# Kernel optimization log

Measured on AMD Instinct MI355X. Metric: run time of the kernel, lower is better.

The kernel has to match this reference:

```python
import jax, jax.numpy as jnp
import numpy as np

N_HEADS = 16
HEAD_DIM = 64
ROPE_BASE = 10000.0


def _rope_cos_sin(T, d, dtype):
    # GPT-NeoX style: inv_freq over even indices, cos/sin duplicated to full head_dim
    inv_freq = 1.0 / (ROPE_BASE ** (jnp.arange(0, d, 2, dtype=jnp.float32) / d))
    freqs = jnp.arange(T, dtype=jnp.float32)[:, None] * inv_freq[None, :]  # [T, d/2]
    emb = jnp.concatenate([freqs, freqs], axis=-1)  # [T, d]
    return jnp.cos(emb).astype(dtype), jnp.sin(emb).astype(dtype)


def _rotate_half(x):
    x1, x2 = jnp.split(x, 2, axis=-1)
    return jnp.concatenate([-x2, x1], axis=-1)


def setup_inputs() -> dict:
    key = jax.random.key(0)
    k1, k2, k3 = jax.random.split(key, 3)
    B, T, C = 2, 2048, 1024
    x = jax.random.normal(k1, (B, T, C), dtype=jnp.float32)
    Wqkv = jax.random.normal(k2, (C, 3 * C), dtype=jnp.float32) * (1.0 / np.sqrt(C))
    Wout = jax.random.normal(k3, (C, C), dtype=jnp.float32) * (1.0 / np.sqrt(C))
    return {"x": x, "Wqkv": Wqkv, "Wout": Wout}


def reference(x, Wqkv, Wout):
    B, T, C = x.shape
    H, D = N_HEADS, HEAD_DIM
    qkv = (x @ Wqkv).reshape(B, T, 3, H, D)
    q, k, v = qkv[:, :, 0], qkv[:, :, 1], qkv[:, :, 2]  # [B,T,H,D]
    q = q.transpose(0, 2, 1, 3)  # [B,H,T,D]
    k = k.transpose(0, 2, 1, 3)
    v = v.transpose(0, 2, 1, 3)
    cos, sin = _rope_cos_sin(T, D, x.dtype)  # [T,D]
    cos = cos[None, None]
    sin = sin[None, None]
    q = q * cos + _rotate_half(q) * sin
    k = k * cos + _rotate_half(k) * sin
    scale = 1.0 / np.sqrt(D)
    scores = jnp.einsum("bhqd,bhkd->bhqk", q, k) * scale  # [B,H,T,T]
    causal = jnp.tril(jnp.ones((T, T), dtype=bool))
    scores = jnp.where(causal[None, None], scores, jnp.finfo(scores.dtype).min)
    attn = jax.nn.softmax(scores, axis=-1)
    out = jnp.einsum("bhqk,bhkd->bhqd", attn, v)  # [B,H,T,D]
    out = out.transpose(0, 2, 1, 3).reshape(B, T, C)
    return out @ Wout
```

## Files before the change

kernel.cpp:

```cpp
#include <hip/hip_runtime.h>


#define B_  2
#define T_  2048
#define C_  1024
#define H_  16
#define D_  64
#define N3_ 3072

typedef unsigned short ushortx8 __attribute__((ext_vector_type(8)));
typedef unsigned short ushortx4 __attribute__((ext_vector_type(4)));
typedef short bf16x8 __attribute__((ext_vector_type(8)));
typedef float f32x4 __attribute__((ext_vector_type(4)));
typedef float f32x16 __attribute__((ext_vector_type(16)));
typedef unsigned int uintx2 __attribute__((ext_vector_type(2)));

__device__ __forceinline__ unsigned short f2bf(float f) {
  union { float f; unsigned u; } v; v.f = f;
  unsigned r = v.u + 0x7FFFu + ((v.u >> 16) & 1u);
  return (unsigned short)(r >> 16);
}
__device__ __forceinline__ float bf2f(unsigned short h) {
  union { unsigned u; float f; } v; v.u = ((unsigned)h) << 16;
  return v.f;
}
__device__ __forceinline__ unsigned cvtpk_bf16(float lo, float hi) {
  unsigned r; asm("v_cvt_pk_bf16_f32 %0, %1, %2" : "=v"(r) : "v"(lo), "v"(hi));
  return r;
}
__device__ __forceinline__ void gload_lds16(const void* g, void* l) {
  __builtin_amdgcn_global_load_lds((const __attribute__((address_space(1))) void*)g,
                                   (__attribute__((address_space(3))) void*)l,
                                   16, 0, 0);
}

__global__ __launch_bounds__(256) void prep_kernel(const float* __restrict__ x,
                                                   unsigned short* __restrict__ Xb,
                                                   const float* __restrict__ Wqkv,
                                                   unsigned short* __restrict__ WqkvT,
                                                   const float* __restrict__ Wout,
                                                   unsigned short* __restrict__ WoutT) {
  __shared__ float tile[32][33];
  const int bid = blockIdx.x;
  if (bid < 4096) {
    size_t i = ((size_t)bid * 256 + threadIdx.x) * 4;
    const float4 v = *(const float4*)(x + i);
    ushortx4 o;
    o[0] = f2bf(v.x); o[1] = f2bf(v.y); o[2] = f2bf(v.z); o[3] = f2bf(v.w);
    *(ushortx4*)(Xb + i) = o;
    return;
  }
  const float* W;
  unsigned short* WT;
  int K, N, n0, k0;
  if (bid < 7168) {
    const int idx = bid - 4096;
    W = Wqkv; WT = WqkvT; K = C_; N = N3_;
    n0 = (idx % (N3_ / 32)) * 32; k0 = (idx / (N3_ / 32)) * 32;
  } else {
    const int idx = bid - 7168;
    W = Wout; WT = WoutT; K = C_; N = C_;
    n0 = (idx % (C_ / 32)) * 32; k0 = (idx / (C_ / 32)) * 32;
  }
  const int tx = threadIdx.x & 31, ty = threadIdx.x >> 5;
#pragma unroll
  for (int i = 0; i < 4; ++i)
    tile[ty + i * 8][tx] = W[(size_t)(k0 + ty + i * 8) * N + n0 + tx];
  __syncthreads();
#pragma unroll
  for (int i = 0; i < 4; ++i)
    WT[(size_t)(n0 + ty + i * 8) * K + k0 + tx] = f2bf(tile[tx][ty + i * 8]);
}

template <int OUTF32>
__global__ __launch_bounds__(256) void gemm_bt_kernel(const unsigned short* __restrict__ A,
                                                      const unsigned short* __restrict__ BT,
                                                      void* __restrict__ Cptr,
                                                      int M, int N, int K) {
  __shared__ unsigned short Alds[128 * 64];
  __shared__ unsigned short Blds[128 * 64];
  const int tid = threadIdx.x;
  const int w = tid >> 6, l = tid & 63;
  const int wr = w >> 1, wc = w & 1;
  const int lg = l >> 4, lr = l & 15;
  const int m0 = blockIdx.y * 128, n0 = blockIdx.x * 128;
  const int lr8 = l >> 3;
  const int lc8 = (l & 7) ^ lr8;

  f32x4 acc[4][4];
#pragma unroll
  for (int i = 0; i < 4; ++i)
#pragma unroll
    for (int j = 0; j < 4; ++j) acc[i][j] = f32x4{0.f, 0.f, 0.f, 0.f};

  for (int k0 = 0; k0 < K; k0 += 64) {
    __syncthreads();
#pragma unroll
    for (int i = 0; i < 4; ++i) {
      const int ch = w * 4 + i;
      gload_lds16(A + (size_t)(m0 + ch * 8 + lr8) * K + k0 + lc8 * 8, &Alds[ch * 512]);
      gload_lds16(BT + (size_t)(n0 + ch * 8 + lr8) * K + k0 + lc8 * 8, &Blds[ch * 512]);
    }
    __syncthreads();
#pragma unroll
    for (int kc = 0; kc < 2; ++kc) {
      bf16x8 af[4], bfr[4];
#pragma unroll
      for (int mi = 0; mi < 4; ++mi) {
        const int row = wr * 64 + mi * 16 + lr;
        const int c16 = (kc * 4 + lg) ^ (row & 7);
        af[mi] = *(const bf16x8*)(&Alds[row * 64 + c16 * 8]);
      }
#pragma unroll
      for (int nj = 0; nj < 4; ++nj) {
        const int row = wc * 64 + nj * 16 + lr;
        const int c16 = (kc * 4 + lg) ^ (row & 7);
        bfr[nj] = *(const bf16x8*)(&Blds[row * 64 + c16 * 8]);
      }
#pragma unroll
      for (int mi = 0; mi < 4; ++mi)
#pragma unroll
        for (int nj = 0; nj < 4; ++nj)
          acc[mi][nj] = __builtin_amdgcn_mfma_f32_16x16x32_bf16(af[mi], bfr[nj], acc[mi][nj], 0, 0, 0);
    }
  }
#pragma unroll
  for (int mi = 0; mi < 4; ++mi)
#pragma unroll
    for (int nj = 0; nj < 4; ++nj)
#pragma unroll
      for (int j = 0; j < 4; ++j) {
        const int row = m0 + wr * 64 + mi * 16 + lg * 4 + j;
        const int col = n0 + wc * 64 + nj * 16 + lr;
        if (OUTF32) ((float*)Cptr)[(size_t)row * N + col] = acc[mi][nj][j];
        else ((unsigned short*)Cptr)[(size_t)row * N + col] = f2bf(acc[mi][nj][j]);
      }
}

__global__ __launch_bounds__(256) void rope_vtrans_kernel(const unsigned short* __restrict__ QKV,
                                                          unsigned short* __restrict__ Qp,
                                                          unsigned short* __restrict__ Kp,
                                                          unsigned short* __restrict__ Vt) {
  __shared__ unsigned short tile[64][72];
  const int tt = blockIdx.x, bh = blockIdx.y;
  const int b = bh >> 4, h = bh & 15;
  const int tid = threadIdx.x;
  if (blockIdx.z == 0) {
    const int half = tid >> 7;
    const int r = (tid >> 1) & 63;
    const int d0 = (tid & 1) * 16;
    const int t = tt * 64 + r;
    const unsigned short* src = QKV + (size_t)(b * T_ + t) * N3_ + half * C_ + h * D_;
    ushortx8 lo0 = *(const ushortx8*)(src + d0);
    ushortx8 lo1 = *(const ushortx8*)(src + d0 + 8);
    ushortx8 hi0 = *(const ushortx8*)(src + d0 + 32);
    ushortx8 hi1 = *(const ushortx8*)(src + d0 + 40);
    ushortx8 olo0, olo1, ohi0, ohi1;
    const float scale = half ? 1.0f : 0.18033688011112042f;
    const float tf = (float)t;
#pragma unroll
    for (int jj = 0; jj < 16; ++jj) {
      const int d = d0 + jj;
      const float invf = exp2f((float)d * -0.41524101186092036f);
      const float ang = tf * invf;
      const float c = cosf(ang), s = sinf(ang);
      const float xl = bf2f(jj < 8 ? lo0[jj] : lo1[jj - 8]);
      const float xh = bf2f(jj < 8 ? hi0[jj] : hi1[jj - 8]);
      const unsigned short rl = f2bf((xl * c - xh * s) * scale);
      const unsigned short rh = f2bf((xh * c + xl * s) * scale);
      if (jj < 8) { olo0[jj] = rl; ohi0[jj] = rh; }
      else        { olo1[jj - 8] = rl; ohi1[jj - 8] = rh; }
    }
    unsigned short* dst = (half ? Kp : Qp) + ((size_t)bh * T_ + t) * D_;
    *(ushortx8*)(dst + d0) = olo0;
    *(ushortx8*)(dst + d0 + 8) = olo1;
    *(ushortx8*)(dst + d0 + 32) = ohi0;
    *(ushortx8*)(dst + d0 + 40) = ohi1;
  } else {
    {
      const int r = tid >> 2, seg = tid & 3;
      const unsigned short* src = QKV + (size_t)(b * T_ + tt * 64 + r) * N3_ + 2 * C_ + h * D_ + seg * 16;
      *(ushortx8*)(&tile[r][seg * 16]) = *(const ushortx8*)(src);
      *(ushortx8*)(&tile[r][seg * 16 + 8]) = *(const ushortx8*)(src + 8);
    }
    __syncthreads();
    {
      const int d = tid >> 2, ts = tid & 3;
      ushortx8 o0, o1;
#pragma unroll
      for (int i = 0; i < 8; ++i) { o0[i] = tile[ts * 16 + i][d]; o1[i] = tile[ts * 16 + 8 + i][d]; }
      unsigned short* dst = Vt + ((size_t)bh * D_ + d) * T_ + tt * 64 + ts * 16;
      *(ushortx8*)(dst) = o0;
      *(ushortx8*)(dst + 8) = o1;
    }
  }
}

__global__ __launch_bounds__(256, 2) void attn9_kernel(const unsigned short* __restrict__ Qp,
                                                       const unsigned short* __restrict__ Kp,
                                                       const unsigned short* __restrict__ Vt,
                                                       unsigned short* __restrict__ Ob) {
  __shared__ unsigned short Klds[3][64 * 64];
  __shared__ unsigned short Vlds[3][64 * 64];
  const int tid = threadIdx.x, w = tid >> 6, l = tid & 63;
  const int lq = l & 31, hi = l >> 5;
  const int swz = lq & 7;
  const int bid = blockIdx.x;
  const int bh = bid & 31;
  const int j = bid >> 5;
  const int g = (j < 8) ? (15 - j) : (j - 8);
  const int s = 4 * g + w;
  const int q0 = s * 32;
  const int ntiles = 2 * g + 2;
  const size_t koff = (size_t)bh * T_ * D_;
  const unsigned short* Kb = Kp + koff;
  const unsigned short* Vb = Vt + (size_t)bh * D_ * T_;

  const int lr8 = l >> 3;
  const int lc8 = (l & 7) ^ lr8;

  bf16x8 qf[4];
  {
    const unsigned short* qp = Qp + koff + (size_t)(q0 + lq) * D_ + hi * 8;
#pragma unroll
    for (int ds = 0; ds < 4; ++ds) qf[ds] = *(const bf16x8*)(qp + ds * 16);
  }
  f32x16 o0, o1;
#pragma unroll
  for (int r = 0; r < 16; ++r) { o0[r] = 0.f; o1[r] = 0.f; }
  float m = -3.0e38f, lden = 0.f;

#pragma unroll
  for (int i = 0; i < 2; ++i) {
    const int c = w * 2 + i;
    gload_lds16(Kb + (size_t)(c * 8 + lr8) * D_ + lc8 * 8, &Klds[0][c * 512]);
    gload_lds16(Vb + (size_t)(c * 8 + lr8) * T_ + lc8 * 8, &Vlds[0][c * 512]);
  }

  for (int kt = 0; kt < ntiles; ++kt) {
    const int cur = kt % 3;
    const int nxt = (kt + 1) % 3;
    const int ktn = (kt + 1 < ntiles) ? kt + 1 : kt;
    const int kvn = ktn * 64;
#pragma unroll
    for (int i = 0; i < 2; ++i) {
      const int c = w * 2 + i;
      gload_lds16(Kb + (size_t)(kvn + c * 8 + lr8) * D_ + lc8 * 8, &Klds[nxt][c * 512]);
      gload_lds16(Vb + (size_t)(c * 8 + lr8) * T_ + kvn + lc8 * 8, &Vlds[nxt][c * 512]);
    }
    asm volatile("s_waitcnt vmcnt(4)" ::: "memory");
    __builtin_amdgcn_s_barrier();
    __builtin_amdgcn_sched_barrier(0);

    const int kv0 = kt * 64;
    if (kv0 <= q0 + 31) {
      const unsigned short* KL = &Klds[cur][0];
      const unsigned short* VL = &Vlds[cur][0];
      f32x16 acc0, acc1;
#pragma unroll
      for (int r = 0; r < 16; ++r) { acc0[r] = 0.f; acc1[r] = 0.f; }
      __builtin_amdgcn_s_setprio(1);
#pragma unroll
      for (int ds = 0; ds < 4; ++ds) {
        const int slot = ((ds * 2 + hi) ^ swz) * 8;
        const bf16x8 kf0 = *(const bf16x8*)(&KL[(lq) * 64 + slot]);
        const bf16x8 kf1 = *(const bf16x8*)(&KL[(32 + lq) * 64 + slot]);
        acc0 = __builtin_amdgcn_mfma_f32_32x32x16_bf16(kf0, qf[ds], acc0, 0, 0, 0);
        acc1 = __builtin_amdgcn_mfma_f32_32x32x16_bf16(kf1, qf[ds], acc1, 0, 0, 0);
      }
      __builtin_amdgcn_s_setprio(0);
      if (kv0 + 63 > q0) {
        const int thr0 = q0 + lq - kv0;
        const int thr1 = thr0 - 32;
#pragma unroll
        for (int r = 0; r < 16; ++r) {
          const int kvloc = (r & 3) + 8 * (r >> 2) + 4 * hi;
          if (kvloc > thr0) acc0[r] = -3.0e38f;
          if (kvloc > thr1) acc1[r] = -3.0e38f;
        }
      }
      float mx[8];
#pragma unroll
      for (int i = 0; i < 8; ++i)
        mx[i] = fmaxf(fmaxf(acc0[i], acc0[i + 8]), fmaxf(acc1[i], acc1[i + 8]));
#pragma unroll
      for (int i = 0; i < 4; ++i) mx[i] = fmaxf(mx[i], mx[i + 4]);
      const float mloc = fmaxf(fmaxf(mx[0], mx[1]), fmaxf(mx[2], mx[3]));
      const uintx2 mp = __builtin_amdgcn_permlane32_swap(__float_as_uint(mloc), __float_as_uint(mloc), false, false);
      const float pm = fmaxf(__uint_as_float(mp.x), __uint_as_float(mp.y));
      const bool grow = pm > m + 8.0f;
      if (__any(grow)) {
        const float mn = grow ? pm : m;
        const float alpha = __builtin_amdgcn_exp2f(m - mn);
        m = mn;
        lden *= alpha;
#pragma unroll
        for (int r = 0; r < 16; ++r) { o0[r] *= alpha; o1[r] *= alpha; }
      }
      float p0[16], p1[16];
#pragma unroll
      for (int r = 0; r < 16; ++r) {
        p0[r] = __builtin_amdgcn_exp2f(acc0[r] - m);
        p1[r] = __builtin_amdgcn_exp2f(acc1[r] - m);
      }
      unsigned W0 = cvtpk_bf16(p0[0], p0[1]), W1 = cvtpk_bf16(p0[2], p0[3]);
      unsigned W2 = cvtpk_bf16(p0[4], p0[5]), W3 = cvtpk_bf16(p0[6], p0[7]);
      uintx2 Aa = __builtin_amdgcn_permlane32_swap(W0, W2, false, false);
      uintx2 Ab = __builtin_amdgcn_permlane32_swap(W1, W3, false, false);
      union { unsigned u[4]; bf16x8 v; } pfa0 = {{Aa.x, Ab.x, Aa.y, Ab.y}};
      W0 = cvtpk_bf16(p0[8], p0[9]);   W1 = cvtpk_bf16(p0[10], p0[11]);
      W2 = cvtpk_bf16(p0[12], p0[13]); W3 = cvtpk_bf16(p0[14], p0[15]);
      Aa = __builtin_amdgcn_permlane32_swap(W0, W2, false, false);
      Ab = __builtin_amdgcn_permlane32_swap(W1, W3, false, false);
      union { unsigned u[4]; bf16x8 v; } pfa1 = {{Aa.x, Ab.x, Aa.y, Ab.y}};
      W0 = cvtpk_bf16(p1[0], p1[1]);   W1 = cvtpk_bf16(p1[2], p1[3]);
      W2 = cvtpk_bf16(p1[4], p1[5]);   W3 = cvtpk_bf16(p1[6], p1[7]);
      Aa = __builtin_amdgcn_permlane32_swap(W0, W2, false, false);
      Ab = __builtin_amdgcn_permlane32_swap(W1, W3, false, false);
      union { unsigned u[4]; bf16x8 v; } pfb0 = {{Aa.x, Ab.x, Aa.y, Ab.y}};
      W0 = cvtpk_bf16(p1[8], p1[9]);   W1 = cvtpk_bf16(p1[10], p1[11]);
      W2 = cvtpk_bf16(p1[12], p1[13]); W3 = cvtpk_bf16(p1[14], p1[15]);
      Aa = __builtin_amdgcn_permlane32_swap(W0, W2, false, false);
      Ab = __builtin_amdgcn_permlane32_swap(W1, W3, false, false);
      union { unsigned u[4]; bf16x8 v; } pfb1 = {{Aa.x, Ab.x, Aa.y, Ab.y}};

      __builtin_amdgcn_s_setprio(1);
#pragma unroll
      for (int dt = 0; dt < 2; ++dt) {
        const int rowb = (dt * 32 + lq) * 64;
        const bf16x8 vf0 = *(const bf16x8*)(&VL[rowb + ((0 * 2 + hi) ^ swz) * 8]);
        const bf16x8 vf1 = *(const bf16x8*)(&VL[rowb + ((1 * 2 + hi) ^ swz) * 8]);
        const bf16x8 vf2 = *(const bf16x8*)(&VL[rowb + ((2 * 2 + hi) ^ swz) * 8]);
        const bf16x8 vf3 = *(const bf16x8*)(&VL[rowb + ((3 * 2 + hi) ^ swz) * 8]);
        if (dt == 0) {
          o0 = __builtin_amdgcn_mfma_f32_32x32x16_bf16(vf0, pfa0.v, o0, 0, 0, 0);
          o0 = __builtin_amdgcn_mfma_f32_32x32x16_bf16(vf1, pfa1.v, o0, 0, 0, 0);
          o0 = __builtin_amdgcn_mfma_f32_32x32x16_bf16(vf2, pfb0.v, o0, 0, 0, 0);
          o0 = __builtin_amdgcn_mfma_f32_32x32x16_bf16(vf3, pfb1.v, o0, 0, 0, 0);
        } else {
          o1 = __builtin_amdgcn_mfma_f32_32x32x16_bf16(vf0, pfa0.v, o1, 0, 0, 0);
          o1 = __builtin_amdgcn_mfma_f32_32x32x16_bf16(vf1, pfa1.v, o1, 0, 0, 0);
          o1 = __builtin_amdgcn_mfma_f32_32x32x16_bf16(vf2, pfb0.v, o1, 0, 0, 0);
          o1 = __builtin_amdgcn_mfma_f32_32x32x16_bf16(vf3, pfb1.v, o1, 0, 0, 0);
        }
      }
      __builtin_amdgcn_s_setprio(0);
      float sm[8];
#pragma unroll
      for (int i = 0; i < 8; ++i) sm[i] = (p0[i] + p0[i + 8]) + (p1[i] + p1[i + 8]);
#pragma unroll
      for (int i = 0; i < 4; ++i) sm[i] = sm[i] + sm[i + 4];
      const float sloc = (sm[0] + sm[1]) + (sm[2] + sm[3]);
      const uintx2 sp = __builtin_amdgcn_permlane32_swap(__float_as_uint(sloc), __float_as_uint(sloc), false, false);
      lden += __uint_as_float(sp.x) + __uint_as_float(sp.y);
    }
  }
  asm volatile("s_waitcnt vmcnt(0)" ::: "memory");

  const float rl = __builtin_amdgcn_rcpf(lden);
  const int b = bh >> 4, hh = bh & 15;
  unsigned short* orow = Ob + (size_t)(b * T_ + q0 + lq) * C_ + hh * D_ + 4 * hi;
#pragma unroll
  for (int rq = 0; rq < 4; ++rq) {
    ushortx4 ov0, ov1;
#pragma unroll
    for (int i = 0; i < 4; ++i) {
      ov0[i] = f2bf(o0[rq * 4 + i] * rl);
      ov1[i] = f2bf(o1[rq * 4 + i] * rl);
    }
    *(ushortx4*)(orow + rq * 8) = ov0;
    *(ushortx4*)(orow + 32 + rq * 8) = ov1;
  }
}

extern "C" void kernel_launch(void* const* d_in, const int* in_sizes, int n_in,
                              void* d_out, int out_size, void* d_ws, size_t ws_size,
                              hipStream_t stream) {
  const float* x = (const float*)d_in[0];
  const float* Wqkv = (const float*)d_in[1];
  const float* Wout = (const float*)d_in[2];
  float* out = (float*)d_out;
  char* ws = (char*)d_ws;
  unsigned short* Xb    = (unsigned short*)(ws);
  unsigned short* WqkvT = (unsigned short*)(ws + (8ull << 20));
  unsigned short* WoutT = (unsigned short*)(ws + (14ull << 20));
  unsigned short* QKVb  = (unsigned short*)(ws + (16ull << 20));
  unsigned short* Qp    = (unsigned short*)(ws + (40ull << 20));
  unsigned short* Kp    = (unsigned short*)(ws + (48ull << 20));
  unsigned short* Vt    = (unsigned short*)(ws + (56ull << 20));
  unsigned short* Ob    = (unsigned short*)(ws + (64ull << 20));

  prep_kernel<<<8192, 256, 0, stream>>>(x, Xb, Wqkv, WqkvT, Wout, WoutT);
  gemm_bt_kernel<0><<<dim3(N3_ / 128, (B_ * T_) / 128), 256, 0, stream>>>(
      Xb, WqkvT, QKVb, B_ * T_, N3_, C_);
  rope_vtrans_kernel<<<dim3(T_ / 64, B_ * H_, 2), 256, 0, stream>>>(QKVb, Qp, Kp, Vt);
  attn9_kernel<<<512, 256, 0, stream>>>(Qp, Kp, Vt, Ob);
  gemm_bt_kernel<1><<<dim3(C_ / 128, (B_ * T_) / 128), 256, 0, stream>>>(
      Ob, WoutT, out, B_ * T_, C_, C_);
}
```

Before: 118.4 us.

## Widen attention KV tiles to 128 with double-buffered LDS staging

The attention kernel now processes 128 keys per iteration instead of 64, with four score accumulators and eight PV MFMAs per step. LDS goes from triple-buffered 64-wide tiles to double-buffered 128-wide tiles, with a new XOR swizzle for the V tile and an extra barrier before each prefetch. This halves the number of loop iterations, softmax reductions and barriers, but drops the per-wave skip of fully masked tiles. Waves whose queries sit early in a 128-key tile now do some wasted masked compute, and register pressure rises.

```diff
diff --git a/kernel.cpp b/kernel.cpp
--- a/kernel.cpp
+++ b/kernel.cpp
@@ -196,12 +196,12 @@
   }
 }
 
-__global__ __launch_bounds__(256, 2) void attn9_kernel(const unsigned short* __restrict__ Qp,
-                                                       const unsigned short* __restrict__ Kp,
-                                                       const unsigned short* __restrict__ Vt,
-                                                       unsigned short* __restrict__ Ob) {
-  __shared__ unsigned short Klds[3][64 * 64];
-  __shared__ unsigned short Vlds[3][64 * 64];
+__global__ __launch_bounds__(256, 2) void attn10_kernel(const unsigned short* __restrict__ Qp,
+                                                        const unsigned short* __restrict__ Kp,
+                                                        const unsigned short* __restrict__ Vt,
+                                                        unsigned short* __restrict__ Ob) {
+  __shared__ unsigned short Klds[2][128 * 64];
+  __shared__ unsigned short Vlds[2][64 * 128];
   const int tid = threadIdx.x, w = tid >> 6, l = tid & 63;
   const int lq = l & 31, hi = l >> 5;
   const int swz = lq & 7;
@@ -209,15 +209,16 @@
   const int bh = bid & 31;
   const int j = bid >> 5;
   const int g = (j < 8) ? (15 - j) : (j - 8);
-  const int s = 4 * g + w;
-  const int q0 = s * 32;
-  const int ntiles = 2 * g + 2;
+  const int q0 = (4 * g + w) * 32;
+  const int nt = g + 1;
   const size_t koff = (size_t)bh * T_ * D_;
   const unsigned short* Kb = Kp + koff;
   const unsigned short* Vb = Vt + (size_t)bh * D_ * T_;
 
   const int lr8 = l >> 3;
   const int lc8 = (l & 7) ^ lr8;
+  const int vrl = l >> 4;
+  const int vsl = l & 15;
 
   bf16x8 qf[4];
   {
@@ -230,130 +231,148 @@
   for (int r = 0; r < 16; ++r) { o0[r] = 0.f; o1[r] = 0.f; }
   float m = -3.0e38f, lden = 0.f;
 
-#pragma unroll
-  for (int i = 0; i < 2; ++i) {
-    const int c = w * 2 + i;
-    gload_lds16(Kb + (size_t)(c * 8 + lr8) * D_ + lc8 * 8, &Klds[0][c * 512]);
-    gload_lds16(Vb + (size_t)(c * 8 + lr8) * T_ + lc8 * 8, &Vlds[0][c * 512]);
-  }
-
-  for (int kt = 0; kt < ntiles; ++kt) {
-    const int cur = kt % 3;
-    const int nxt = (kt + 1) % 3;
-    const int ktn = (kt + 1 < ntiles) ? kt + 1 : kt;
-    const int kvn = ktn * 64;
-#pragma unroll
-    for (int i = 0; i < 2; ++i) {
-      const int c = w * 2 + i;
-      gload_lds16(Kb + (size_t)(kvn + c * 8 + lr8) * D_ + lc8 * 8, &Klds[nxt][c * 512]);
-      gload_lds16(Vb + (size_t)(c * 8 + lr8) * T_ + kvn + lc8 * 8, &Vlds[nxt][c * 512]);
-    }
-    asm volatile("s_waitcnt vmcnt(4)" ::: "memory");
+  auto stage = [&](int buf, int kv0s) {
+#pragma unroll
+    for (int i = 0; i < 4; ++i) {
+      const int c = w * 4 + i;
+      gload_lds16(Kb + (size_t)(kv0s + c * 8 + lr8) * D_ + lc8 * 8, &Klds[buf][c * 512]);
+    }
+#pragma unroll
+    for (int i = 0; i < 4; ++i) {
+      const int c = w * 4 + i;
+      const int vr = c * 4 + vrl;
+      const int vs = vsl ^ (vr & 7);
+      gload_lds16(Vb + (size_t)vr * T_ + kv0s + vs * 8, &Vlds[buf][c * 512]);
+    }
+  };
+  auto pack2 = [&](const f32x16& p, bf16x8& fa, bf16x8& fb) {
+    unsigned W0 = cvtpk_bf16(p[0], p[1]), W1 = cvtpk_bf16(p[2], p[3]);
+    unsigned W2 = cvtpk_bf16(p[4], p[5]), W3 = cvtpk_bf16(p[6], p[7]);
+    uintx2 Aa = __builtin_amdgcn_permlane32_swap(W0, W2, false, false);
+    uintx2 Ab = __builtin_amdgcn_permlane32_swap(W1, W3, false, false);
+    union { unsigned u[4]; bf16x8 v; } t1 = {{Aa.x, Ab.x, Aa.y, Ab.y}};
+    fa = t1.v;
+    W0 = cvtpk_bf16(p[8], p[9]);   W1 = cvtpk_bf16(p[10], p[11]);
+    W2 = cvtpk_bf16(p[12], p[13]); W3 = cvtpk_bf16(p[14], p[15]);
+    Aa = __builtin_amdgcn_permlane32_swap(W0, W2, false, false);
+    Ab = __builtin_amdgcn_permlane32_swap(W1, W3, false, false);
+    union { unsigned u[4]; bf16x8 v; } t2 = {{Aa.x, Ab.x, Aa.y, Ab.y}};
+    fb = t2.v;
+  };
+
+  stage(0, 0);
+
+  for (int kt = 0; kt < nt; ++kt) {
+    const int cur = kt & 1, nxt = cur ^ 1;
+    __builtin_amdgcn_s_barrier();
+    const int ktn = (kt + 1 < nt) ? kt + 1 : kt;
+    stage(nxt, ktn * 128);
+    asm volatile("s_waitcnt vmcnt(8)" ::: "memory");
     __builtin_amdgcn_s_barrier();
     __builtin_amdgcn_sched_barrier(0);
 
-    const int kv0 = kt * 64;
-    if (kv0 <= q0 + 31) {
-      const unsigned short* KL = &Klds[cur][0];
-      const unsigned short* VL = &Vlds[cur][0];
-      f32x16 acc0, acc1;
-#pragma unroll
-      for (int r = 0; r < 16; ++r) { acc0[r] = 0.f; acc1[r] = 0.f; }
-      __builtin_amdgcn_s_setprio(1);
-#pragma unroll
-      for (int ds = 0; ds < 4; ++ds) {
-        const int slot = ((ds * 2 + hi) ^ swz) * 8;
-        const bf16x8 kf0 = *(const bf16x8*)(&KL[(lq) * 64 + slot]);
-        const bf16x8 kf1 = *(const bf16x8*)(&KL[(32 + lq) * 64 + slot]);
-        acc0 = __builtin_amdgcn_mfma_f32_32x32x16_bf16(kf0, qf[ds], acc0, 0, 0, 0);
-        acc1 = __builtin_amdgcn_mfma_f32_32x32x16_bf16(kf1, qf[ds], acc1, 0, 0, 0);
+    const unsigned short* KL = &Klds[cur][0];
+    const unsigned short* VL = &Vlds[cur][0];
+    const int kv0 = kt * 128;
+    f32x16 a0, a1, a2, a3;
+#pragma unroll
+    for (int r = 0; r < 16; ++r) { a0[r] = 0.f; a1[r] = 0.f; a2[r] = 0.f; a3[r] = 0.f; }
+    __builtin_amdgcn_s_setprio(1);
+#pragma unroll
+    for (int ds = 0; ds < 4; ++ds) {
+      const int slot = ((ds * 2 + hi) ^ swz) * 8;
+      const bf16x8 k0f = *(const bf16x8*)(&KL[(lq) * 64 + slot]);
+      const bf16x8 k1f = *(const bf16x8*)(&KL[(32 + lq) * 64 + slot]);
+      const bf16x8 k2f = *(const bf16x8*)(&KL[(64 + lq) * 64 + slot]);
+      const bf16x8 k3f = *(const bf16x8*)(&KL[(96 + lq) * 64 + slot]);
+      a0 = __builtin_amdgcn_mfma_f32_32x32x16_bf16(k0f, qf[ds], a0, 0, 0, 0);
+      a1 = __builtin_amdgcn_mfma_f32_32x32x16_bf16(k1f, qf[ds], a1, 0, 0, 0);
+      a2 = __builtin_amdgcn_mfma_f32_32x32x16_bf16(k2f, qf[ds], a2, 0, 0, 0);
+      a3 = __builtin_amdgcn_mfma_f32_32x32x16_bf16(k3f, qf[ds], a3, 0, 0, 0);
+    }
+    __builtin_amdgcn_s_setprio(0);
+    if (kv0 + 127 > q0) {
+      const int thr = q0 + lq - kv0;
+#pragma unroll
+      for (int r = 0; r < 16; ++r) {
+        const int kvloc = (r & 3) + 8 * (r >> 2) + 4 * hi;
+        if (kvloc > thr)      a0[r] = -3.0e38f;
+        if (kvloc > thr - 32) a1[r] = -3.0e38f;
+        if (kvloc > thr - 64) a2[r] = -3.0e38f;
+        if (kvloc > thr - 96) a3[r] = -3.0e38f;
       }
-      __builtin_amdgcn_s_setprio(0);
-      if (kv0 + 63 > q0) {
-        const int thr0 = q0 + lq - kv0;
-        const int thr1 = thr0 - 32;
-#pragma unroll
-        for (int r = 0; r < 16; ++r) {
-          const int kvloc = (r & 3) + 8 * (r >> 2) + 4 * hi;
-          if (kvloc > thr0) acc0[r] = -3.0e38f;
-          if (kvloc > thr1) acc1[r] = -3.0e38f;
-        }
+    }
+    float mx[8];
+#pragma unroll
+    for (int i = 0; i < 8; ++i)
+      mx[i] = fmaxf(fmaxf(fmaxf(a0[i], a0[i + 8]), fmaxf(a1[i], a1[i + 8])),
+                    fmaxf(fmaxf(a2[i], a2[i + 8]), fmaxf(a3[i], a3[i + 8])));
+#pragma unroll
+    for (int i = 0; i < 4; ++i) mx[i] = fmaxf(mx[i], mx[i + 4]);
+    const float mloc = fmaxf(fmaxf(mx[0], mx[1]), fmaxf(mx[2], mx[3]));
+    const uintx2 mp = __builtin_amdgcn_permlane32_swap(__float_as_uint(mloc), __float_as_uint(mloc), false, false);
+    const float pm = fmaxf(__uint_as_float(mp.x), __uint_as_float(mp.y));
+    const bool grow = pm > m + 8.0f;
+    if (__any(grow)) {
+      const float mn = grow ? pm : m;
+      const float alpha = __builtin_amdgcn_exp2f(m - mn);
+      m = mn;
+      lden *= alpha;
+#pragma unroll
+      for (int r = 0; r < 16; ++r) { o0[r] *= alpha; o1[r] *= alpha; }
+    }
+#pragma unroll
+    for (int r = 0; r < 16; ++r) {
+      a0[r] = __builtin_amdgcn_exp2f(a0[r] - m);
+      a1[r] = __builtin_amdgcn_exp2f(a1[r] - m);
+      a2[r] = __builtin_amdgcn_exp2f(a2[r] - m);
+      a3[r] = __builtin_amdgcn_exp2f(a3[r] - m);
+    }
+    bf16x8 f0, f1, f2, f3, f4, f5, f6, f7;
+    pack2(a0, f0, f1); pack2(a1, f2, f3); pack2(a2, f4, f5); pack2(a3, f6, f7);
+    __builtin_amdgcn_s_setprio(1);
+#pragma unroll
+    for (int dt = 0; dt < 2; ++dt) {
+      const int rowb = (dt * 32 + lq) * 128;
+      const bf16x8 v0 = *(const bf16x8*)(&VL[rowb + ((0 * 2 + hi) ^ swz) * 8]);
+      const bf16x8 v1 = *(const bf16x8*)(&VL[rowb + ((1 * 2 + hi) ^ swz) * 8]);
+      const bf16x8 v2 = *(const bf16x8*)(&VL[rowb + ((2 * 2 + hi) ^ swz) * 8]);
+      const bf16x8 v3 = *(const bf16x8*)(&VL[rowb + ((3 * 2 + hi) ^ swz) * 8]);
+      const bf16x8 v4 = *(const bf16x8*)(&VL[rowb + ((4 * 2 + hi) ^ swz) * 8]);
+      const bf16x8 v5 = *(const bf16x8*)(&VL[rowb + ((5 * 2 + hi) ^ swz) * 8]);
+      const bf16x8 v6 = *(const bf16x8*)(&VL[rowb + ((6 * 2 + hi) ^ swz) * 8]);
+      const bf16x8 v7 = *(const bf16x8*)(&VL[rowb + ((7 * 2 + hi) ^ swz) * 8]);
+      if (dt == 0) {
+        o0 = __builtin_amdgcn_mfma_f32_32x32x16_bf16(v0, f0, o0, 0, 0, 0);
+        o0 = __builtin_amdgcn_mfma_f32_32x32x16_bf16(v1, f1, o0, 0, 0, 0);
+        o0 = __builtin_amdgcn_mfma_f32_32x32x16_bf16(v2, f2, o0, 0, 0, 0);
+        o0 = __builtin_amdgcn_mfma_f32_32x32x16_bf16(v3, f3, o0, 0, 0, 0);
+        o0 = __builtin_amdgcn_mfma_f32_32x32x16_bf16(v4, f4, o0, 0, 0, 0);
+        o0 = __builtin_amdgcn_mfma_f32_32x32x16_bf16(v5, f5, o0, 0, 0, 0);
+        o0 = __builtin_amdgcn_mfma_f32_32x32x16_bf16(v6, f6, o0, 0, 0, 0);
+        o0 = __builtin_amdgcn_mfma_f32_32x32x16_bf16(v7, f7, o0, 0, 0, 0);
+      } else {
+        o1 = __builtin_amdgcn_mfma_f32_32x32x16_bf16(v0, f0, o1, 0, 0, 0);
+        o1 = __builtin_amdgcn_mfma_f32_32x32x16_bf16(v1, f1, o1, 0, 0, 0);
+        o1 = __builtin_amdgcn_mfma_f32_32x32x16_bf16(v2, f2, o1, 0, 0, 0);
+        o1 = __builtin_amdgcn_mfma_f32_32x32x16_bf16(v3, f3, o1, 0, 0, 0);
+        o1 = __builtin_amdgcn_mfma_f32_32x32x16_bf16(v4, f4, o1, 0, 0, 0);
+        o1 = __builtin_amdgcn_mfma_f32_32x32x16_bf16(v5, f5, o1, 0, 0, 0);
+        o1 = __builtin_amdgcn_mfma_f32_32x32x16_bf16(v6, f6, o1, 0, 0, 0);
+        o1 = __builtin_amdgcn_mfma_f32_32x32x16_bf16(v7, f7, o1, 0, 0, 0);
       }
-      float mx[8];
-#pragma unroll
-      for (int i = 0; i < 8; ++i)
-        mx[i] = fmaxf(fmaxf(acc0[i], acc0[i + 8]), fmaxf(acc1[i], acc1[i + 8]));
-#pragma unroll
-      for (int i = 0; i < 4; ++i) mx[i] = fmaxf(mx[i], mx[i + 4]);
-      const float mloc = fmaxf(fmaxf(mx[0], mx[1]), fmaxf(mx[2], mx[3]));
-      const uintx2 mp = __builtin_amdgcn_permlane32_swap(__float_as_uint(mloc), __float_as_uint(mloc), false, false);
-      const float pm = fmaxf(__uint_as_float(mp.x), __uint_as_float(mp.y));
-      const bool grow = pm > m + 8.0f;
-      if (__any(grow)) {
-        const float mn = grow ? pm : m;
-        const float alpha = __builtin_amdgcn_exp2f(m - mn);
-        m = mn;
-        lden *= alpha;
-#pragma unroll
-        for (int r = 0; r < 16; ++r) { o0[r] *= alpha; o1[r] *= alpha; }
-      }
-      float p0[16], p1[16];
-#pragma unroll
-      for (int r = 0; r < 16; ++r) {
-        p0[r] = __builtin_amdgcn_exp2f(acc0[r] - m);
-        p1[r] = __builtin_amdgcn_exp2f(acc1[r] - m);
-      }
-      unsigned W0 = cvtpk_bf16(p0[0], p0[1]), W1 = cvtpk_bf16(p0[2], p0[3]);
-      unsigned W2 = cvtpk_bf16(p0[4], p0[5]), W3 = cvtpk_bf16(p0[6], p0[7]);
-      uintx2 Aa = __builtin_amdgcn_permlane32_swap(W0, W2, false, false);
-      uintx2 Ab = __builtin_amdgcn_permlane32_swap(W1, W3, false, false);
-      union { unsigned u[4]; bf16x8 v; } pfa0 = {{Aa.x, Ab.x, Aa.y, Ab.y}};
-      W0 = cvtpk_bf16(p0[8], p0[9]);   W1 = cvtpk_bf16(p0[10], p0[11]);
-      W2 = cvtpk_bf16(p0[12], p0[13]); W3 = cvtpk_bf16(p0[14], p0[15]);
-      Aa = __builtin_amdgcn_permlane32_swap(W0, W2, false, false);
-      Ab = __builtin_amdgcn_permlane32_swap(W1, W3, false, false);
-      union { unsigned u[4]; bf16x8 v; } pfa1 = {{Aa.x, Ab.x, Aa.y, Ab.y}};
-      W0 = cvtpk_bf16(p1[0], p1[1]);   W1 = cvtpk_bf16(p1[2], p1[3]);
-      W2 = cvtpk_bf16(p1[4], p1[5]);   W3 = cvtpk_bf16(p1[6], p1[7]);
-      Aa = __builtin_amdgcn_permlane32_swap(W0, W2, false, false);
-      Ab = __builtin_amdgcn_permlane32_swap(W1, W3, false, false);
-      union { unsigned u[4]; bf16x8 v; } pfb0 = {{Aa.x, Ab.x, Aa.y, Ab.y}};
-      W0 = cvtpk_bf16(p1[8], p1[9]);   W1 = cvtpk_bf16(p1[10], p1[11]);
-      W2 = cvtpk_bf16(p1[12], p1[13]); W3 = cvtpk_bf16(p1[14], p1[15]);
-      Aa = __builtin_amdgcn_permlane32_swap(W0, W2, false, false);
-      Ab = __builtin_amdgcn_permlane32_swap(W1, W3, false, false);
-      union { unsigned u[4]; bf16x8 v; } pfb1 = {{Aa.x, Ab.x, Aa.y, Ab.y}};
-
-      __builtin_amdgcn_s_setprio(1);
-#pragma unroll
-      for (int dt = 0; dt < 2; ++dt) {
-        const int rowb = (dt * 32 + lq) * 64;
-        const bf16x8 vf0 = *(const bf16x8*)(&VL[rowb + ((0 * 2 + hi) ^ swz) * 8]);
-        const bf16x8 vf1 = *(const bf16x8*)(&VL[rowb + ((1 * 2 + hi) ^ swz) * 8]);
-        const bf16x8 vf2 = *(const bf16x8*)(&VL[rowb + ((2 * 2 + hi) ^ swz) * 8]);
-        const bf16x8 vf3 = *(const bf16x8*)(&VL[rowb + ((3 * 2 + hi) ^ swz) * 8]);
-        if (dt == 0) {
-          o0 = __builtin_amdgcn_mfma_f32_32x32x16_bf16(vf0, pfa0.v, o0, 0, 0, 0);
-          o0 = __builtin_amdgcn_mfma_f32_32x32x16_bf16(vf1, pfa1.v, o0, 0, 0, 0);
-          o0 = __builtin_amdgcn_mfma_f32_32x32x16_bf16(vf2, pfb0.v, o0, 0, 0, 0);
-          o0 = __builtin_amdgcn_mfma_f32_32x32x16_bf16(vf3, pfb1.v, o0, 0, 0, 0);
-        } else {
-          o1 = __builtin_amdgcn_mfma_f32_32x32x16_bf16(vf0, pfa0.v, o1, 0, 0, 0);
-          o1 = __builtin_amdgcn_mfma_f32_32x32x16_bf16(vf1, pfa1.v, o1, 0, 0, 0);
-          o1 = __builtin_amdgcn_mfma_f32_32x32x16_bf16(vf2, pfb0.v, o1, 0, 0, 0);
-          o1 = __builtin_amdgcn_mfma_f32_32x32x16_bf16(vf3, pfb1.v, o1, 0, 0, 0);
-        }
-      }
-      __builtin_amdgcn_s_setprio(0);
-      float sm[8];
-#pragma unroll
-      for (int i = 0; i < 8; ++i) sm[i] = (p0[i] + p0[i + 8]) + (p1[i] + p1[i + 8]);
-#pragma unroll
-      for (int i = 0; i < 4; ++i) sm[i] = sm[i] + sm[i + 4];
-      const float sloc = (sm[0] + sm[1]) + (sm[2] + sm[3]);
-      const uintx2 sp = __builtin_amdgcn_permlane32_swap(__float_as_uint(sloc), __float_as_uint(sloc), false, false);
-      lden += __uint_as_float(sp.x) + __uint_as_float(sp.y);
-    }
+    }
+    __builtin_amdgcn_s_setprio(0);
+    float sm[8];
+#pragma unroll
+    for (int i = 0; i < 8; ++i)
+      sm[i] = ((a0[i] + a0[i + 8]) + (a1[i] + a1[i + 8])) +
+              ((a2[i] + a2[i + 8]) + (a3[i] + a3[i + 8]));
+#pragma unroll
+    for (int i = 0; i < 4; ++i) sm[i] = sm[i] + sm[i + 4];
+    const float sloc = (sm[0] + sm[1]) + (sm[2] + sm[3]);
+    const uintx2 sp = __builtin_amdgcn_permlane32_swap(__float_as_uint(sloc), __float_as_uint(sloc), false, false);
+    lden += __uint_as_float(sp.x) + __uint_as_float(sp.y);
   }
   asm volatile("s_waitcnt vmcnt(0)" ::: "memory");
 
@@ -394,7 +413,7 @@
   gemm_bt_kernel<0><<<dim3(N3_ / 128, (B_ * T_) / 128), 256, 0, stream>>>(
       Xb, WqkvT, QKVb, B_ * T_, N3_, C_);
   rope_vtrans_kernel<<<dim3(T_ / 64, B_ * H_, 2), 256, 0, stream>>>(QKVb, Qp, Kp, Vt);
-  attn9_kernel<<<512, 256, 0, stream>>>(Qp, Kp, Vt, Ob);
+  attn10_kernel<<<512, 256, 0, stream>>>(Qp, Kp, Vt, Ob);
   gemm_bt_kernel<1><<<dim3(C_ / 128, (B_ * T_) / 128), 256, 0, stream>>>(
       Ob, WoutT, out, B_ * T_, C_, C_);
 }
```

Result: faster. 114.9 us (-2.9%).
